# Optimization experiments

Measured on AMD Instinct MI355X. Metric: run time of the kernel, lower is better.

## Reference

```python
import jax, jax.numpy as jnp
import numpy as np

B, S, D = 4, 4096, 1024

def setup_inputs() -> dict:
    key = jax.random.key(0)
    ks = jax.random.split(key, 7)
    scale = 1.0 / np.sqrt(D)
    X  = jax.random.normal(ks[0], (B, S, D), dtype=jnp.float32)
    Wq = jax.random.normal(ks[1], (D, D), dtype=jnp.float32) * scale
    bq = jnp.zeros((D,), dtype=jnp.float32)
    Wk = jax.random.normal(ks[2], (D, D), dtype=jnp.float32) * scale
    bk = jnp.zeros((D,), dtype=jnp.float32)
    Wv = jax.random.normal(ks[3], (D, D), dtype=jnp.float32) * scale
    bv = jnp.zeros((D,), dtype=jnp.float32)
    return {"X": X, "Wq": Wq, "bq": bq, "Wk": Wk, "bk": bk, "Wv": Wv, "bv": bv}

def reference(X, Wq, bq, Wk, bk, Wv, bv):
    # Linear projections (torch Linear: x @ W.T + b; here W stored as [D_in, D_out])
    Q = jnp.einsum('bsd,de->bse', X, Wq) + bq
    K = jnp.einsum('bsd,de->bse', X, Wk) + bk
    V = jnp.einsum('bsd,de->bse', X, Wv) + bv
    inv_sqrt_d = 1.0 / jnp.sqrt(jnp.float32(X.shape[-1]))
    scores = jnp.einsum('bqd,bkd->bqk', Q, K) * inv_sqrt_d  # [B,S,S]
    weights = jax.nn.sigmoid(scores)  # elementwise, no row normalization
    return jnp.einsum('bqk,bkd->bqd', weights, V)
```

## Files before the change

kernel.cpp:

```cpp
#include <hip/hip_runtime.h>
#include <hip/hip_bf16.h>

typedef __bf16 bf16_t;
typedef bf16_t bf16x8 __attribute__((ext_vector_type(8)));
typedef float f32x4 __attribute__((ext_vector_type(4)));

constexpr int D_DIM = 1024;
constexpr int S_DIM = 4096;
constexpr int B_DIM = 4;

__global__ void cast_f32_bf16(const float* __restrict__ in, bf16_t* __restrict__ out) {
  size_t i = ((size_t)blockIdx.x * blockDim.x + threadIdx.x) * 8;
  float4 a = *(const float4*)(in + i);
  float4 b = *(const float4*)(in + i + 4);
  bf16x8 o;
  o[0] = (bf16_t)a.x; o[1] = (bf16_t)a.y; o[2] = (bf16_t)a.z; o[3] = (bf16_t)a.w;
  o[4] = (bf16_t)b.x; o[5] = (bf16_t)b.y; o[6] = (bf16_t)b.z; o[7] = (bf16_t)b.w;
  *(bf16x8*)(out + i) = o;
}

__global__ void transpose_cast_1024(const float* __restrict__ in, bf16_t* __restrict__ out) {
  __shared__ float t[32][33];
  int x0 = blockIdx.x * 32, y0 = blockIdx.y * 32;
#pragma unroll
  for (int i = 0; i < 32; i += 8)
    t[threadIdx.y + i][threadIdx.x] =
        in[(size_t)(y0 + threadIdx.y + i) * D_DIM + (x0 + threadIdx.x)];
  __syncthreads();
#pragma unroll
  for (int i = 0; i < 32; i += 8)
    out[(size_t)(x0 + threadIdx.y + i) * D_DIM + (y0 + threadIdx.x)] =
        (bf16_t)t[threadIdx.x][threadIdx.y + i];
}

constexpr int BM2 = 256, BN2 = 256;

#define VMCNT4 asm volatile("s_waitcnt vmcnt(4)" ::: "memory")
#define VMCNT2 asm volatile("s_waitcnt vmcnt(2)" ::: "memory")
#define VMCNT0 asm volatile("s_waitcnt vmcnt(0)" ::: "memory")
#define LGKM8  asm volatile("s_waitcnt lgkmcnt(8)" ::: "memory")
#define LGKM0  asm volatile("s_waitcnt lgkmcnt(0)" ::: "memory")
#define SCHEDB __builtin_amdgcn_sched_barrier(0)
#define CFENCE asm volatile("" ::: "memory")
#define BAR __builtin_amdgcn_s_barrier()
#define PRIO1 __builtin_amdgcn_s_setprio(1)
#define PRIO0 __builtin_amdgcn_s_setprio(0)

__device__ __forceinline__ void stage_half(const bf16_t* __restrict__ g, int ld,
                                           char* lds, int tid) {
  const int w = tid >> 6, l = tid & 63;
  const int rw = l >> 3;
  const int gl = (l & 7) ^ rw;
  char* l0 = lds + w * 1024;
  const bf16_t* s0 = g + (size_t)(w * 8 + rw) * ld + gl * 8;
  __builtin_amdgcn_global_load_lds((const __attribute__((address_space(1))) void*)s0,
                                   (__attribute__((address_space(3))) void*)l0, 16, 0, 0);
  __builtin_amdgcn_global_load_lds(
      (const __attribute__((address_space(1))) void*)(s0 + (size_t)64 * ld),
      (__attribute__((address_space(3))) void*)(l0 + 8192), 16, 0, 0);
}

__device__ __forceinline__ void load_a4(const char* __restrict__ At, int wr, int fm, int s,
                                        int kxa, int kxb, bf16x8 (&af)[4][2]) {
#pragma unroll
  for (int m = 0; m < 4; ++m) {
    const char* p = At + (wr + (s * 4 + m) * 16 + fm) * 128;
    af[m][0] = *(const bf16x8*)(p + kxa);
    af[m][1] = *(const bf16x8*)(p + kxb);
  }
}

__device__ __forceinline__ void load_b2(const char* __restrict__ Bt_, int wc, int fm, int n0,
                                        int kxa, int kxb, bf16x8 (&bfr)[4][2]) {
#pragma unroll
  for (int n = n0; n < n0 + 2; ++n) {
    const char* p = Bt_ + (wc + n * 16 + fm) * 128;
    bfr[n][0] = *(const bf16x8*)(p + kxa);
    bfr[n][1] = *(const bf16x8*)(p + kxb);
  }
}

__device__ __forceinline__ void mfma_q(f32x4 (&acc)[8][4], const bf16x8 (&af)[4][2],
                                       const bf16x8 (&bfr)[4][2], int ms, int ns) {
#pragma unroll
  for (int kh = 0; kh < 2; ++kh)
#pragma unroll
    for (int m = 0; m < 4; ++m)
#pragma unroll
      for (int n = 0; n < 2; ++n)
        acc[ms * 4 + m][ns * 2 + n] = __builtin_amdgcn_mfma_f32_16x16x32_bf16(
            af[m][kh], bfr[ns * 2 + n][kh], acc[ms * 4 + m][ns * 2 + n], 0, 0, 0);
}

template <int EPI, bool SWAP>
__global__ __launch_bounds__(512, 2) void gemm256(
    const bf16_t* __restrict__ A, const bf16_t* __restrict__ Bt,
    void* __restrict__ C0, void* __restrict__ C1, void* __restrict__ C2,
    const float* __restrict__ b0, const float* __restrict__ b1, const float* __restrict__ b2,
    int K, int lda, int ldb, int ldc, float scale,
    size_t sA, size_t sB, size_t sC) {
  __shared__ __align__(16) char smem[131072];
  char* const A0t = smem;
  char* const B0t = smem + 32768;
  char* const A1t = smem + 65536;
  char* const B1t = smem + 98304;

  const int tid = threadIdx.x;
  const int lane = tid & 63;
  const int w = tid >> 6;
  const int wr = (w >> 2) * 128;
  const int wc = (w & 3) * 64;
  const int fm = lane & 15;
  const int ssw = (fm & 7) << 4;
  const int kp = (lane >> 4) << 4;
  const int kxa = kp ^ ssw;
  const int kxb = (64 | kp) ^ ssw;

  const int nx = gridDim.x, ny = gridDim.y;
  const int nwg = nx * ny * gridDim.z;
  const int flat = blockIdx.x + nx * (blockIdx.y + ny * blockIdx.z);
  const int q = nwg >> 3;
  const int L = (flat & 7) * q + (flat >> 3);
  const int lx = L % nx;
  const int lt = L / nx;
  const int ly = lt % ny;
  const int lz = lt / ny;

  const int bx = SWAP ? ly : lx;
  const int by = SWAP ? lx : ly;

  const bf16_t* Ag = A + (size_t)lz * sA + (size_t)by * BM2 * lda;
  const bf16_t* Bg = Bt + (size_t)lz * sB + (size_t)bx * BN2 * ldb;

  f32x4 acc[8][4] = {};
  bf16x8 af[4][2], bfr[4][2];

  const int NI = K / 128;

  stage_half(Ag, lda, A0t, tid);
  stage_half(Ag + (size_t)128 * lda, lda, A0t + 16384, tid);
  stage_half(Bg, ldb, B0t, tid);
  stage_half(Bg + (size_t)128 * ldb, ldb, B0t + 16384, tid);
  stage_half(Bg + 64, ldb, B1t, tid);
  stage_half(Bg + 64 + (size_t)128 * ldb, ldb, B1t + 16384, tid);
  VMCNT4;
  BAR;

  for (int it = 0; it < NI; ++it) {
    const bool last = (it == NI - 1);
    const bf16_t* Ao  = Ag + (size_t)(2 * it + 1) * 64;
    const bf16_t* Ae2 = Ag + (size_t)(2 * it + 2) * 64;
    const bf16_t* Be2 = Bg + (size_t)(2 * it + 2) * 64;
    const bf16_t* Bo2 = Bg + (size_t)(2 * it + 3) * 64;

    load_a4(A0t, wr, fm, 0, kxa, kxb, af);
    load_b2(B0t, wc, fm, 0, kxa, kxb, bfr);
    stage_half(Ao, lda, A1t, tid);
    LGKM8; CFENCE; BAR;
    LGKM0; SCHEDB;
    PRIO1; mfma_q(acc, af, bfr, 0, 0); PRIO0;
    BAR;

    load_a4(A0t, wr, fm, 1, kxa, kxb, af);
    stage_half(Ao + (size_t)128 * lda, lda, A1t + 16384, tid);
    CFENCE; BAR;
    LGKM0; SCHEDB;
    PRIO1; mfma_q(acc, af, bfr, 1, 0); PRIO0;
    BAR;

    load_b2(B0t, wc, fm, 2, kxa, kxb, bfr);
    CFENCE; BAR;
    LGKM0; SCHEDB;
    PRIO1; mfma_q(acc, af, bfr, 1, 1); PRIO0;
    BAR;

    load_a4(A0t, wr, fm, 0, kxa, kxb, af);
    if (!last) stage_half(Be2, ldb, B0t, tid);
    CFENCE; BAR;
    LGKM0; SCHEDB;
    PRIO1; mfma_q(acc, af, bfr, 0, 1); PRIO0;
    if (last) { VMCNT0; } else { VMCNT2; }
    BAR;

    load_a4(A1t, wr, fm, 0, kxa, kxb, af);
    load_b2(B1t, wc, fm, 0, kxa, kxb, bfr);
    if (!last) {
      stage_half(Be2 + (size_t)128 * ldb, ldb, B0t + 16384, tid);
      stage_half(Ae2, lda, A0t, tid);
    }
    LGKM8; CFENCE; BAR;
    LGKM0; SCHEDB;
    PRIO1; mfma_q(acc, af, bfr, 0, 0); PRIO0;
    BAR;

    load_a4(A1t, wr, fm, 1, kxa, kxb, af);
    if (!last) stage_half(Ae2 + (size_t)128 * lda, lda, A0t + 16384, tid);
    CFENCE; BAR;
    LGKM0; SCHEDB;
    PRIO1; mfma_q(acc, af, bfr, 1, 0); PRIO0;
    BAR;

    load_b2(B1t, wc, fm, 2, kxa, kxb, bfr);
    CFENCE; BAR;
    LGKM0; SCHEDB;
    PRIO1; mfma_q(acc, af, bfr, 1, 1); PRIO0;
    BAR;

    load_a4(A1t, wr, fm, 0, kxa, kxb, af);
    if (!last) {
      stage_half(Bo2, ldb, B1t, tid);
      stage_half(Bo2 + (size_t)128 * ldb, ldb, B1t + 16384, tid);
    }
    CFENCE; BAR;
    LGKM0; SCHEDB;
    PRIO1; mfma_q(acc, af, bfr, 0, 1); PRIO0;
    if (!last) { VMCNT4; }
    BAR;
  }

  const int row0 = by * BM2 + wr + (lane >> 4) * 4;
  const int col0 = bx * BN2 + wc + fm;

  if constexpr (EPI == 0) {
    const int seg = bx >> 2;
    const float* bias = (seg == 0) ? b0 : (seg == 1) ? b1 : b2;
#pragma unroll
    for (int i = 0; i < 8; ++i) {
#pragma unroll
      for (int j = 0; j < 4; ++j) {
        const int n = col0 + j * 16;
        const int nl = n & 1023;
        const float bv = bias[nl];
#pragma unroll
        for (int r = 0; r < 4; ++r) {
          const int m = row0 + i * 16 + r;
          float v = acc[i][j][r] + bv;
          if (seg < 2) {
            bf16_t* C = (bf16_t*)(seg == 0 ? C0 : C1);
            C[(size_t)m * D_DIM + nl] = (bf16_t)v;
          } else {
            bf16_t* C = (bf16_t*)C2;
            C[((size_t)(m >> 12) << 22) + (size_t)nl * S_DIM + (m & (S_DIM - 1))] = (bf16_t)v;
          }
        }
      }
    }
  } else {
#pragma unroll
    for (int i = 0; i < 8; ++i) {
#pragma unroll
      for (int j = 0; j < 4; ++j) {
        const int n = col0 + j * 16;
#pragma unroll
        for (int r = 0; r < 4; ++r) {
          const int m = row0 + i * 16 + r;
          float v = acc[i][j][r];
          if constexpr (EPI == 2) {
            bf16_t* C = (bf16_t*)C0 + (size_t)lz * sC;
            float s = 1.0f / (1.0f + __expf(-v * scale));
            C[(size_t)m * ldc + n] = (bf16_t)s;
          } else {
            float* C = (float*)C0 + (size_t)lz * sC;
            C[(size_t)m * ldc + n] = v;
          }
        }
      }
    }
  }
}

extern "C" void kernel_launch(void* const* d_in, const int* in_sizes, int n_in,
                              void* d_out, int out_size, void* d_ws, size_t ws_size,
                              hipStream_t stream) {
  const float* X  = (const float*)d_in[0];
  const float* Wq = (const float*)d_in[1];
  const float* bq = (const float*)d_in[2];
  const float* Wk = (const float*)d_in[3];
  const float* bk = (const float*)d_in[4];
  const float* Wv = (const float*)d_in[5];
  const float* bv = (const float*)d_in[6];
  float* out = (float*)d_out;

  const int M = B_DIM * S_DIM;
  const size_t SD = (size_t)S_DIM * D_DIM;
  const size_t E  = (size_t)M * D_DIM;
  const size_t PE1 = (size_t)S_DIM * S_DIM;
  const size_t WE = (size_t)D_DIM * D_DIM;

  size_t need4 = (4 * PE1 + 3 * E + 3 * WE) * sizeof(bf16_t);
  const int PB = (ws_size >= need4) ? 4 : 1;
  const size_t psz = (size_t)PB * PE1;

  bf16_t* ws = (bf16_t*)d_ws;
  bf16_t* P   = ws;
  bf16_t* Xb  = ws;
  bf16_t* Qb  = ws + psz;
  bf16_t* Kb  = Qb + E;
  bf16_t* Vt  = Kb + E;
  bf16_t* Wt  = Vt + E;

  cast_f32_bf16<<<dim3((unsigned)(E / 8 / 256)), dim3(256), 0, stream>>>(X, Xb);

  dim3 tg(D_DIM / 32, D_DIM / 32), tb(32, 8);
  transpose_cast_1024<<<tg, tb, 0, stream>>>(Wq, Wt);
  transpose_cast_1024<<<tg, tb, 0, stream>>>(Wk, Wt + WE);
  transpose_cast_1024<<<tg, tb, 0, stream>>>(Wv, Wt + 2 * WE);

  dim3 pg(3 * D_DIM / BN2, M / BM2, 1);
  gemm256<0, false><<<pg, dim3(512), 0, stream>>>(
      Xb, Wt, Qb, Kb, Vt, bq, bk, bv, D_DIM, D_DIM, D_DIM, D_DIM, 1.0f, 0, 0, 0);

  const float scale = 0.03125f;
  for (int b0 = 0; b0 < B_DIM; b0 += PB) {
    dim3 sg(S_DIM / BN2, S_DIM / BM2, PB);
    gemm256<2, false><<<sg, dim3(512), 0, stream>>>(
        Qb + (size_t)b0 * SD, Kb + (size_t)b0 * SD, P,
        nullptr, nullptr, nullptr, nullptr, nullptr,
        D_DIM, D_DIM, D_DIM, S_DIM, scale, SD, SD, PE1);
    dim3 vg(S_DIM / BM2, D_DIM / BN2, PB);
    gemm256<3, true><<<vg, dim3(512), 0, stream>>>(
        P, Vt + (size_t)b0 * SD, out + (size_t)b0 * SD,
        nullptr, nullptr, nullptr, nullptr, nullptr,
        S_DIM, S_DIM, S_DIM, D_DIM, 1.0f, PE1, SD, SD);
  }
}
```

Baseline: 535.6 us.

## Use a 16-wave 1024-thread GEMM variant for the QKV projection

Adds a dedicated QKV projection kernel that runs 1024 threads (16 waves) per 256x256 tile. Each wave now owns a 64x64 sub-tile instead of 128x64, so it holds half the accumulators and A fragments. Each wave stages only one 16-byte row slice per half-tile. The goal is more waves in flight to hide LDS and global latency in the projection GEMM. The cost is more barrier participants per workgroup and a changed wait-count schedule. The generic gemm256 template loses its bias/QKV epilogue and extra arguments.

```diff
diff --git a/kernel.cpp b/kernel.cpp
--- a/kernel.cpp
+++ b/kernel.cpp
@@ -37,6 +37,7 @@
 
 #define VMCNT4 asm volatile("s_waitcnt vmcnt(4)" ::: "memory")
 #define VMCNT2 asm volatile("s_waitcnt vmcnt(2)" ::: "memory")
+#define VMCNT1 asm volatile("s_waitcnt vmcnt(1)" ::: "memory")
 #define VMCNT0 asm volatile("s_waitcnt vmcnt(0)" ::: "memory")
 #define LGKM8  asm volatile("s_waitcnt lgkmcnt(8)" ::: "memory")
 #define LGKM0  asm volatile("s_waitcnt lgkmcnt(0)" ::: "memory")
@@ -60,6 +61,17 @@
       (__attribute__((address_space(3))) void*)(l0 + 8192), 16, 0, 0);
 }
 
+__device__ __forceinline__ void stage_half16(const bf16_t* __restrict__ g, int ld,
+                                             char* lds, int tid) {
+  const int w = tid >> 6, l = tid & 63;
+  const int rw = l >> 3;
+  const int gl = (l & 7) ^ rw;
+  char* l0 = lds + w * 1024;
+  const bf16_t* s0 = g + (size_t)(w * 8 + rw) * ld + gl * 8;
+  __builtin_amdgcn_global_load_lds((const __attribute__((address_space(1))) void*)s0,
+                                   (__attribute__((address_space(3))) void*)l0, 16, 0, 0);
+}
+
 __device__ __forceinline__ void load_a4(const char* __restrict__ At, int wr, int fm, int s,
                                         int kxa, int kxb, bf16x8 (&af)[4][2]) {
 #pragma unroll
@@ -70,6 +82,16 @@
   }
 }
 
+__device__ __forceinline__ void load_a2(const char* __restrict__ At, int wr, int fm, int s,
+                                        int kxa, int kxb, bf16x8 (&af)[2][2]) {
+#pragma unroll
+  for (int m = 0; m < 2; ++m) {
+    const char* p = At + (wr + (s * 2 + m) * 16 + fm) * 128;
+    af[m][0] = *(const bf16x8*)(p + kxa);
+    af[m][1] = *(const bf16x8*)(p + kxb);
+  }
+}
+
 __device__ __forceinline__ void load_b2(const char* __restrict__ Bt_, int wc, int fm, int n0,
                                         int kxa, int kxb, bf16x8 (&bfr)[4][2]) {
 #pragma unroll
@@ -92,11 +114,22 @@
             af[m][kh], bfr[ns * 2 + n][kh], acc[ms * 4 + m][ns * 2 + n], 0, 0, 0);
 }
 
+__device__ __forceinline__ void mfma_q16(f32x4 (&acc)[4][4], const bf16x8 (&af)[2][2],
+                                         const bf16x8 (&bfr)[4][2], int ms, int ns) {
+#pragma unroll
+  for (int kh = 0; kh < 2; ++kh)
+#pragma unroll
+    for (int m = 0; m < 2; ++m)
+#pragma unroll
+      for (int n = 0; n < 2; ++n)
+        acc[ms * 2 + m][ns * 2 + n] = __builtin_amdgcn_mfma_f32_16x16x32_bf16(
+            af[m][kh], bfr[ns * 2 + n][kh], acc[ms * 2 + m][ns * 2 + n], 0, 0, 0);
+}
+
 template <int EPI, bool SWAP>
 __global__ __launch_bounds__(512, 2) void gemm256(
     const bf16_t* __restrict__ A, const bf16_t* __restrict__ Bt,
-    void* __restrict__ C0, void* __restrict__ C1, void* __restrict__ C2,
-    const float* __restrict__ b0, const float* __restrict__ b1, const float* __restrict__ b2,
+    void* __restrict__ C0,
     int K, int lda, int ldb, int ldc, float scale,
     size_t sA, size_t sB, size_t sC) {
   __shared__ __align__(16) char smem[131072];
@@ -221,48 +254,167 @@
   const int row0 = by * BM2 + wr + (lane >> 4) * 4;
   const int col0 = bx * BN2 + wc + fm;
 
-  if constexpr (EPI == 0) {
-    const int seg = bx >> 2;
-    const float* bias = (seg == 0) ? b0 : (seg == 1) ? b1 : b2;
-#pragma unroll
-    for (int i = 0; i < 8; ++i) {
-#pragma unroll
-      for (int j = 0; j < 4; ++j) {
-        const int n = col0 + j * 16;
-        const int nl = n & 1023;
-        const float bv = bias[nl];
-#pragma unroll
-        for (int r = 0; r < 4; ++r) {
-          const int m = row0 + i * 16 + r;
-          float v = acc[i][j][r] + bv;
-          if (seg < 2) {
-            bf16_t* C = (bf16_t*)(seg == 0 ? C0 : C1);
-            C[(size_t)m * D_DIM + nl] = (bf16_t)v;
-          } else {
-            bf16_t* C = (bf16_t*)C2;
-            C[((size_t)(m >> 12) << 22) + (size_t)nl * S_DIM + (m & (S_DIM - 1))] = (bf16_t)v;
-          }
+#pragma unroll
+  for (int i = 0; i < 8; ++i) {
+#pragma unroll
+    for (int j = 0; j < 4; ++j) {
+      const int n = col0 + j * 16;
+#pragma unroll
+      for (int r = 0; r < 4; ++r) {
+        const int m = row0 + i * 16 + r;
+        float v = acc[i][j][r];
+        if constexpr (EPI == 2) {
+          bf16_t* C = (bf16_t*)C0 + (size_t)lz * sC;
+          float s = 1.0f / (1.0f + __expf(-v * scale));
+          C[(size_t)m * ldc + n] = (bf16_t)s;
+        } else {
+          float* C = (float*)C0 + (size_t)lz * sC;
+          C[(size_t)m * ldc + n] = v;
         }
       }
     }
-  } else {
-#pragma unroll
-    for (int i = 0; i < 8; ++i) {
-#pragma unroll
-      for (int j = 0; j < 4; ++j) {
-        const int n = col0 + j * 16;
-#pragma unroll
-        for (int r = 0; r < 4; ++r) {
-          const int m = row0 + i * 16 + r;
-          float v = acc[i][j][r];
-          if constexpr (EPI == 2) {
-            bf16_t* C = (bf16_t*)C0 + (size_t)lz * sC;
-            float s = 1.0f / (1.0f + __expf(-v * scale));
-            C[(size_t)m * ldc + n] = (bf16_t)s;
-          } else {
-            float* C = (float*)C0 + (size_t)lz * sC;
-            C[(size_t)m * ldc + n] = v;
-          }
+  }
+}
+
+__global__ __launch_bounds__(1024, 4) void gemm256_w16_qkv(
+    const bf16_t* __restrict__ A, const bf16_t* __restrict__ Bt,
+    bf16_t* __restrict__ Cq, bf16_t* __restrict__ Ck, bf16_t* __restrict__ Cv,
+    const float* __restrict__ b0, const float* __restrict__ b1, const float* __restrict__ b2,
+    int lda, int ldb) {
+  __shared__ __align__(16) char smem[131072];
+  char* const A0t = smem;
+  char* const B0t = smem + 32768;
+  char* const A1t = smem + 65536;
+  char* const B1t = smem + 98304;
+
+  const int tid = threadIdx.x;
+  const int lane = tid & 63;
+  const int w = tid >> 6;
+  const int wr = (w >> 2) * 64;
+  const int wc = (w & 3) * 64;
+  const int fm = lane & 15;
+  const int ssw = (fm & 7) << 4;
+  const int kp = (lane >> 4) << 4;
+  const int kxa = kp ^ ssw;
+  const int kxb = (64 | kp) ^ ssw;
+
+  const int nx = gridDim.x, ny = gridDim.y;
+  const int nwg = nx * ny;
+  const int flat = blockIdx.x + nx * blockIdx.y;
+  const int q = nwg >> 3;
+  const int L = (flat & 7) * q + (flat >> 3);
+  const int bx = L % nx;
+  const int by = L / nx;
+
+  const bf16_t* Ag = A + (size_t)by * BM2 * lda;
+  const bf16_t* Bg = Bt + (size_t)bx * BN2 * ldb;
+
+  f32x4 acc[4][4] = {};
+  bf16x8 af[2][2], bfr[4][2];
+
+  const int NI = D_DIM / 128;
+
+  stage_half16(Ag, lda, A0t, tid);
+  stage_half16(Ag + (size_t)128 * lda, lda, A0t + 16384, tid);
+  stage_half16(Bg, ldb, B0t, tid);
+  stage_half16(Bg + (size_t)128 * ldb, ldb, B0t + 16384, tid);
+  stage_half16(Bg + 64, ldb, B1t, tid);
+  stage_half16(Bg + 64 + (size_t)128 * ldb, ldb, B1t + 16384, tid);
+  VMCNT2;
+  BAR;
+
+  for (int it = 0; it < NI; ++it) {
+    const bool last = (it == NI - 1);
+    const bf16_t* Ao  = Ag + (size_t)(2 * it + 1) * 64;
+    const bf16_t* Ae2 = Ag + (size_t)(2 * it + 2) * 64;
+    const bf16_t* Be2 = Bg + (size_t)(2 * it + 2) * 64;
+    const bf16_t* Bo2 = Bg + (size_t)(2 * it + 3) * 64;
+
+    load_a2(A0t, wr, fm, 0, kxa, kxb, af);
+    load_b2(B0t, wc, fm, 0, kxa, kxb, bfr);
+    stage_half16(Ao, lda, A1t, tid);
+    CFENCE; BAR;
+    LGKM0; SCHEDB;
+    PRIO1; mfma_q16(acc, af, bfr, 0, 0); PRIO0;
+    BAR;
+
+    load_a2(A0t, wr, fm, 1, kxa, kxb, af);
+    stage_half16(Ao + (size_t)128 * lda, lda, A1t + 16384, tid);
+    CFENCE; BAR;
+    LGKM0; SCHEDB;
+    PRIO1; mfma_q16(acc, af, bfr, 1, 0); PRIO0;
+    BAR;
+
+    load_b2(B0t, wc, fm, 2, kxa, kxb, bfr);
+    CFENCE; BAR;
+    LGKM0; SCHEDB;
+    PRIO1; mfma_q16(acc, af, bfr, 1, 1); PRIO0;
+    BAR;
+
+    load_a2(A0t, wr, fm, 0, kxa, kxb, af);
+    if (!last) stage_half16(Be2, ldb, B0t, tid);
+    CFENCE; BAR;
+    LGKM0; SCHEDB;
+    PRIO1; mfma_q16(acc, af, bfr, 0, 1); PRIO0;
+    if (last) { VMCNT0; } else { VMCNT1; }
+    BAR;
+
+    load_a2(A1t, wr, fm, 0, kxa, kxb, af);
+    load_b2(B1t, wc, fm, 0, kxa, kxb, bfr);
+    if (!last) {
+      stage_half16(Be2 + (size_t)128 * ldb, ldb, B0t + 16384, tid);
+      stage_half16(Ae2, lda, A0t, tid);
+    }
+    CFENCE; BAR;
+    LGKM0; SCHEDB;
+    PRIO1; mfma_q16(acc, af, bfr, 0, 0); PRIO0;
+    BAR;
+
+    load_a2(A1t, wr, fm, 1, kxa, kxb, af);
+    if (!last) stage_half16(Ae2 + (size_t)128 * lda, lda, A0t + 16384, tid);
+    CFENCE; BAR;
+    LGKM0; SCHEDB;
+    PRIO1; mfma_q16(acc, af, bfr, 1, 0); PRIO0;
+    BAR;
+
+    load_b2(B1t, wc, fm, 2, kxa, kxb, bfr);
+    CFENCE; BAR;
+    LGKM0; SCHEDB;
+    PRIO1; mfma_q16(acc, af, bfr, 1, 1); PRIO0;
+    BAR;
+
+    load_a2(A1t, wr, fm, 0, kxa, kxb, af);
+    if (!last) {
+      stage_half16(Bo2, ldb, B1t, tid);
+      stage_half16(Bo2 + (size_t)128 * ldb, ldb, B1t + 16384, tid);
+    }
+    CFENCE; BAR;
+    LGKM0; SCHEDB;
+    PRIO1; mfma_q16(acc, af, bfr, 0, 1); PRIO0;
+    if (!last) { VMCNT2; }
+    BAR;
+  }
+
+  const int row0 = by * BM2 + wr + (lane >> 4) * 4;
+  const int col0 = bx * BN2 + wc + fm;
+  const int seg = bx >> 2;
+  const float* bias = (seg == 0) ? b0 : (seg == 1) ? b1 : b2;
+#pragma unroll
+  for (int i = 0; i < 4; ++i) {
+#pragma unroll
+    for (int j = 0; j < 4; ++j) {
+      const int n = col0 + j * 16;
+      const int nl = n & 1023;
+      const float bv = bias[nl];
+#pragma unroll
+      for (int r = 0; r < 4; ++r) {
+        const int m = row0 + i * 16 + r;
+        float v = acc[i][j][r] + bv;
+        if (seg < 2) {
+          bf16_t* C = (seg == 0) ? Cq : Ck;
+          C[(size_t)m * D_DIM + nl] = (bf16_t)v;
+        } else {
+          Cv[((size_t)(m >> 12) << 22) + (size_t)nl * S_DIM + (m & (S_DIM - 1))] = (bf16_t)v;
         }
       }
     }
@@ -307,20 +459,18 @@
   transpose_cast_1024<<<tg, tb, 0, stream>>>(Wv, Wt + 2 * WE);
 
   dim3 pg(3 * D_DIM / BN2, M / BM2, 1);
-  gemm256<0, false><<<pg, dim3(512), 0, stream>>>(
-      Xb, Wt, Qb, Kb, Vt, bq, bk, bv, D_DIM, D_DIM, D_DIM, D_DIM, 1.0f, 0, 0, 0);
+  gemm256_w16_qkv<<<pg, dim3(1024), 0, stream>>>(
+      Xb, Wt, Qb, Kb, Vt, bq, bk, bv, D_DIM, D_DIM);
 
   const float scale = 0.03125f;
   for (int b0 = 0; b0 < B_DIM; b0 += PB) {
     dim3 sg(S_DIM / BN2, S_DIM / BM2, PB);
     gemm256<2, false><<<sg, dim3(512), 0, stream>>>(
         Qb + (size_t)b0 * SD, Kb + (size_t)b0 * SD, P,
-        nullptr, nullptr, nullptr, nullptr, nullptr,
         D_DIM, D_DIM, D_DIM, S_DIM, scale, SD, SD, PE1);
     dim3 vg(S_DIM / BM2, D_DIM / BN2, PB);
     gemm256<3, true><<<vg, dim3(512), 0, stream>>>(
         P, Vt + (size_t)b0 * SD, out + (size_t)b0 * SD,
-        nullptr, nullptr, nullptr, nullptr, nullptr,
         S_DIM, S_DIM, S_DIM, D_DIM, 1.0f, PE1, SD, SD);
   }
 }
```

New measurement: 568.9 us. 1.06x slower.
